# Kernel optimization log

Hardware: AMD Instinct MI355X
Metric: run time of the kernel (lower is better)

## Reference

```python
import jax, jax.numpy as jnp
import numpy as np

B, S, DIN, DOUT = 4, 2048, 4096, 4096

def setup_inputs() -> dict:
    key = jax.random.key(0)
    k1, k2, k3, k4 = jax.random.split(key, 4)
    x = jax.random.normal(k1, (B, S, DIN), dtype=jnp.float32)
    # symmetric int8 weight values in [-127, 127]
    quantized_weight = jax.random.randint(k2, (DOUT, DIN), -127, 128, dtype=jnp.int32).astype(jnp.int8)
    weight_scale = jax.random.uniform(k3, (), dtype=jnp.float32) * 0.01 + 1e-4
    bias = jax.random.normal(k4, (DOUT,), dtype=jnp.float32)
    return {"x": x, "quantized_weight": quantized_weight, "weight_scale": weight_scale, "bias": bias}

def reference(x, quantized_weight, weight_scale, bias) -> jnp.ndarray:
    # dequantize_tensor: (q.float() - 0) * scale
    weight_fp32 = quantized_weight.astype(jnp.float32) * weight_scale  # [DOUT, DIN]
    # nn.functional.linear: x @ W^T + b
    return jnp.einsum('bsi,oi->bso', x, weight_fp32) + bias
```

## Files before the change

kernel.cpp:

```cpp
#include <hip/hip_runtime.h>
#include <stdint.h>
#include <stddef.h>

constexpr int MDIM = 8192;
constexpr int NDIM = 4096;
constexpr int KDIM = 4096;

using f32x4 = __attribute__((ext_vector_type(4))) float;
using s16x4 = __attribute__((ext_vector_type(4))) short;
using s16x8 = __attribute__((ext_vector_type(8))) short;
using i32x4 = __attribute__((ext_vector_type(4))) int;

__device__ __forceinline__ short f32_to_bf16_rn(float f) {
  union { float f; uint32_t u; } v; v.f = f;
  uint32_t r = (v.u + 0x7FFFu + ((v.u >> 16) & 1u)) >> 16;
  return (short)(uint16_t)r;
}

__global__ void __launch_bounds__(256) quant_x_kernel(const float* __restrict__ in,
                                                      signed char* __restrict__ out,
                                                      float* __restrict__ sx) {
  const int row = blockIdx.x;
  const int t   = threadIdx.x;
  const float* rp = in + (size_t)row * KDIM;
  f32x4 v[4];
  float m = 0.0f;
#pragma unroll
  for (int j = 0; j < 4; ++j) {
    v[j] = *(const f32x4*)(rp + t * 16 + j * 4);
#pragma unroll
    for (int e = 0; e < 4; ++e) m = fmaxf(m, __builtin_fabsf(v[j][e]));
  }
#pragma unroll
  for (int off = 32; off > 0; off >>= 1) m = fmaxf(m, __shfl_xor(m, off, 64));
  __shared__ float wmax[4];
  const int wv = t >> 6, ln = t & 63;
  if (ln == 0) wmax[wv] = m;
  __syncthreads();
  m = fmaxf(fmaxf(wmax[0], wmax[1]), fmaxf(wmax[2], wmax[3]));
  const float inv = (m > 0.0f) ? (127.0f / m) : 0.0f;
  if (t == 0) sx[row] = m * (1.0f / 127.0f);
  i32x4 o;
#pragma unroll
  for (int j = 0; j < 4; ++j) {
    int b[4];
#pragma unroll
    for (int e = 0; e < 4; ++e) {
      int q = (int)rintf(v[j][e] * inv);
      q = q < -127 ? -127 : (q > 127 ? 127 : q);
      b[e] = q & 255;
    }
    o[j] = b[0] | (b[1] << 8) | (b[2] << 16) | (b[3] << 24);
  }
  *(i32x4*)(out + (size_t)row * KDIM + t * 16) = o;
}

__global__ void __launch_bounds__(256) quant_w_kernel(const int* __restrict__ in,
                                                      signed char* __restrict__ out, int n16) {
  int i = blockIdx.x * 256 + threadIdx.x;
  const int stride = gridDim.x * 256;
  for (; i < n16; i += stride) {
    const i32x4* p = (const i32x4*)(in + (size_t)i * 16);
    i32x4 o;
#pragma unroll
    for (int j = 0; j < 4; ++j) {
      i32x4 a = p[j];
      o[j] = (a[0] & 255) | ((a[1] & 255) << 8) | ((a[2] & 255) << 16) | ((a[3] & 255) << 24);
    }
    *(i32x4*)(out + (size_t)i * 16) = o;
  }
}


#define BAR asm volatile("s_barrier" ::: "memory")
#define WAITVM(n) asm volatile("s_waitcnt vmcnt(" #n ")" ::: "memory")

#define GLL(src, dst) __builtin_amdgcn_global_load_lds(                     \
    (const __attribute__((address_space(1))) void*)(src),                   \
    (__attribute__((address_space(3))) void*)(dst), 16, 0, 0)

#define STGP(tau) do {                                                      \
  GLL(Arow + (size_t)r0 * 4096 + (tau) * 64 + cb,                           \
      lds + (tau) * 32768 + t * 16);                                        \
  GLL(Arow + (size_t)(128 + r0) * 4096 + (tau) * 64 + cb,                   \
      lds + (tau) * 32768 + 8192 + t * 16);                                 \
  GLL(Brow + (size_t)r0 * 4096 + (tau) * 64 + cb,                           \
      lds + (tau) * 32768 + 16384 + t * 16);                                \
  GLL(Brow + (size_t)(128 + r0) * 4096 + (tau) * 64 + cb,                   \
      lds + (tau) * 32768 + 16384 + 8192 + t * 16);                         \
} while (0)

#define STGL(u3) do {                                                       \
  GLL(aSrc0, lds + (u3) * 32768 + t * 16);                                  \
  GLL(aSrc1, lds + (u3) * 32768 + 8192 + t * 16);                           \
  GLL(bSrc0, lds + (u3) * 32768 + 16384 + t * 16);                          \
  GLL(bSrc1, lds + (u3) * 32768 + 16384 + 8192 + t * 16);                   \
  aSrc0 += 64; aSrc1 += 64; bSrc0 += 64; bSrc1 += 64;                       \
} while (0)

#define LDA8(u, fi) (*(const i32x4*)(lds + (u) * 32768                      \
    + (wm * 8 + (fi)) * 1024 + laneoff))
#define LDB8(u, j)  (*(const i32x4*)(lds + (u) * 32768 + 16384              \
    + (wn * 4 + (j)) * 1024 + laneoff))

#define WIN(u, AFC, BFC, AFN, BFN, dord, dostg, vmarg) do {                 \
  if (dord) {                                                               \
    _Pragma("unroll") for (int i_ = 0; i_ < 8; ++i_)                        \
      AFN[i_] = LDA8(((u) + 1) & 3, i_);                                    \
    _Pragma("unroll") for (int j_ = 0; j_ < 4; ++j_)                        \
      BFN[j_] = LDB8(((u) + 1) & 3, j_);                                    \
  }                                                                         \
  if (dostg) STGL(((u) + 3) & 3);                                           \
  __builtin_amdgcn_s_setprio(1);                                            \
  _Pragma("unroll") for (int i_ = 0; i_ < 8; ++i_)                          \
  _Pragma("unroll") for (int j_ = 0; j_ < 4; ++j_)                          \
    acc[i_][j_] = __builtin_amdgcn_mfma_i32_16x16x64_i8(                    \
        AFC[i_], BFC[j_], acc[i_][j_], 0, 0, 0);                            \
  __builtin_amdgcn_s_setprio(0);                                            \
  if ((vmarg) == 4) { WAITVM(4); } else if ((vmarg) == 0) { WAITVM(0); }    \
  BAR;                                                                      \
} while (0)

__global__ void __launch_bounds__(512, 1) gemm_i8_ring(
    const signed char* __restrict__ A, const signed char* __restrict__ Bw,
    const float* __restrict__ sx, const float* __restrict__ scale_p,
    const float* __restrict__ bias, float* __restrict__ out) {
  __shared__ __align__(16) char lds[131072];

  const int t      = threadIdx.x;
  const int lane   = t & 63;
  const int wave   = t >> 6;
  const int wm     = wave >> 2;
  const int wn     = wave & 3;
  const int lane15 = lane & 15;
  const int lh     = lane >> 4;

  const int laneoff = (lane15 * 64 + lh * 16) ^ ((lane15 & 8) << 2);

  const int ax = ((t >> 5) & 1) << 5;
  const int a0 = (t * 16) ^ ax;
  const int r0 = a0 >> 6;
  const int cb = a0 & 63;

  const int bid   = blockIdx.x;
  const int wg    = (bid & 7) * 64 + (bid >> 3);
  const int ntile = wg & 15;
  const int mtile = wg >> 4;
  const int m0 = mtile * 256;
  const int n0 = ntile * 256;

  const char* Arow = (const char*)(A + (size_t)m0 * KDIM);
  const char* Brow = (const char*)(Bw + (size_t)n0 * KDIM);

  const char* aSrc0 = Arow + (size_t)r0 * 4096 + 192 + cb;
  const char* aSrc1 = Arow + (size_t)(128 + r0) * 4096 + 192 + cb;
  const char* bSrc0 = Brow + (size_t)r0 * 4096 + 192 + cb;
  const char* bSrc1 = Brow + (size_t)(128 + r0) * 4096 + 192 + cb;

  i32x4 acc[8][4] = {};
  i32x4 afE[8], afO[8], bfE[4], bfO[4];

  STGP(0);
  STGP(1);
  STGP(2);
  WAITVM(8);
  BAR;
#pragma unroll
  for (int i_ = 0; i_ < 8; ++i_) afE[i_] = LDA8(0, i_);
#pragma unroll
  for (int j_ = 0; j_ < 4; ++j_) bfE[j_] = LDB8(0, j_);
  WAITVM(4);
  BAR;

#pragma unroll 1
  for (int tp = 0; tp < 15; ++tp) {
    WIN(0, afE, bfE, afO, bfO, 1, 1, 4);
    WIN(1, afO, bfO, afE, bfE, 1, 1, 4);
    WIN(2, afE, bfE, afO, bfO, 1, 1, 4);
    WIN(3, afO, bfO, afE, bfE, 1, 1, 4);
  }
  WIN(0, afE, bfE, afO, bfO, 1, 1, 4);
  WIN(1, afO, bfO, afE, bfE, 1, 0, 0);
  WIN(2, afE, bfE, afO, bfO, 1, 0, -1);
  WIN(3, afO, bfO, afE, bfE, 0, 0, -1);

  const float sw = scale_p[0];
  float bv[4];
#pragma unroll
  for (int j = 0; j < 4; ++j) bv[j] = bias[n0 + wn * 64 + j * 16 + lane15];
#pragma unroll
  for (int i = 0; i < 8; ++i) {
    const int rowb = m0 + wm * 128 + i * 16 + lh * 4;
    float sxq[4];
#pragma unroll
    for (int q = 0; q < 4; ++q) sxq[q] = sx[rowb + q] * sw;
#pragma unroll
    for (int j = 0; j < 4; ++j) {
      const int col = n0 + wn * 64 + j * 16 + lane15;
#pragma unroll
      for (int q = 0; q < 4; ++q)
        out[(size_t)(rowb + q) * NDIM + col] = (float)acc[i][j][q] * sxq[q] + bv[j];
    }
  }
}

constexpr int FTILE = 128;
constexpr int FBK   = 64;

__global__ void __launch_bounds__(256) gemm_raw(
    const float* __restrict__ X, const int* __restrict__ W,
    const float* __restrict__ scale_p, const float* __restrict__ bias,
    float* __restrict__ out) {
  __shared__ short As[FTILE * FBK];
  __shared__ short Bs[FTILE * FBK];

  const int t      = threadIdx.x;
  const int lane   = t & 63;
  const int wave   = t >> 6;
  const int wm     = wave >> 1;
  const int wn     = wave & 1;
  const int lane15   = lane & 15;
  const int laneHalf = lane >> 4;

  const int bid   = blockIdx.x;
  const int wg    = (bid & 7) * 256 + (bid >> 3);
  const int ntile = wg & 31;
  const int mtile = wg >> 5;
  const int m0 = mtile * FTILE;
  const int n0 = ntile * FTILE;

  f32x4 acc[4][4] = {};

  for (int k0 = 0; k0 < KDIM; k0 += FBK) {
    __syncthreads();
#pragma unroll
    for (int r = 0; r < 8; ++r) {
      const int f   = r * 256 + t;
      const int row = f >> 4;
      const int c4  = (f & 15) * 4;
      f32x4 v = *(const f32x4*)(X + (size_t)(m0 + row) * KDIM + (k0 + c4));
      s16x4 h;
#pragma unroll
      for (int j = 0; j < 4; ++j) h[j] = f32_to_bf16_rn(v[j]);
      *(s16x4*)&As[row * FBK + c4] = h;

      i32x4 wv = *(const i32x4*)(W + (size_t)(n0 + row) * KDIM + (k0 + c4));
      s16x4 hw;
#pragma unroll
      for (int j = 0; j < 4; ++j) hw[j] = f32_to_bf16_rn((float)wv[j]);
      *(s16x4*)&Bs[row * FBK + c4] = hw;
    }
    __syncthreads();

#pragma unroll
    for (int kk = 0; kk < FBK; kk += 32) {
      const int kb = kk + laneHalf * 8;
      s16x8 af[4], bf[4];
#pragma unroll
      for (int i = 0; i < 4; ++i) {
        af[i] = *(const s16x8*)&As[(wm * 64 + i * 16 + lane15) * FBK + kb];
        bf[i] = *(const s16x8*)&Bs[(wn * 64 + i * 16 + lane15) * FBK + kb];
      }
#pragma unroll
      for (int i = 0; i < 4; ++i)
#pragma unroll
        for (int j = 0; j < 4; ++j)
          acc[i][j] = __builtin_amdgcn_mfma_f32_16x16x32_bf16(af[i], bf[j], acc[i][j], 0, 0, 0);
    }
  }

  const float s = scale_p[0];
#pragma unroll
  for (int j = 0; j < 4; ++j) {
    const int col = n0 + wn * 64 + j * 16 + lane15;
    const float bv = bias[col];
#pragma unroll
    for (int i = 0; i < 4; ++i) {
      const int row = m0 + wm * 64 + i * 16 + laneHalf * 4;
#pragma unroll
      for (int q = 0; q < 4; ++q)
        out[(size_t)(row + q) * NDIM + col] = acc[i][j][q] * s + bv;
    }
  }
}

extern "C" void kernel_launch(void* const* d_in, const int* in_sizes, int n_in,
                              void* d_out, int out_size, void* d_ws, size_t ws_size,
                              hipStream_t stream) {
  const float* x     = (const float*)d_in[0];
  const int*   w     = (const int*)d_in[1];
  const float* scale = (const float*)d_in[2];
  const float* bias  = (const float*)d_in[3];
  float* out = (float*)d_out;

  const size_t a_bytes = (size_t)MDIM * KDIM;
  const size_t b_bytes = (size_t)NDIM * KDIM;
  const size_t need    = a_bytes + b_bytes + MDIM * 4;

  if (ws_size >= need) {
    signed char* Ai8 = (signed char*)d_ws;
    signed char* Bi8 = Ai8 + a_bytes;
    float*       sxp = (float*)(Bi8 + b_bytes);
    quant_x_kernel<<<MDIM, 256, 0, stream>>>(x, Ai8, sxp);
    quant_w_kernel<<<4096, 256, 0, stream>>>(w, Bi8, (int)(b_bytes / 16));
    const int nwg = (MDIM / 256) * (NDIM / 256);
    gemm_i8_ring<<<nwg, 512, 0, stream>>>(Ai8, Bi8, sxp, scale, bias, out);
  } else {
    const int nwg = (MDIM / FTILE) * (NDIM / FTILE);
    gemm_raw<<<nwg, 256, 0, stream>>>(x, w, scale, bias, out);
  }
}
```

Before: 186.8 us.

## Switch int8 GEMM to 32x32x32 MFMA with new LDS swizzle layout

Replaces the 16x16x64 int8 MFMA tiling with 32x32x32 int8 MFMA, so each wave computes a 4x2 grid of 32x32 fragments with i32x16 accumulators split over two K sub-steps. The LDS staging addresses and XOR swizzle are redone for 32-row fragments, and the epilogue is rewritten for the 32x32 output register layout. The intent is fewer MFMA issues and fewer LDS fragment reads per unit of work, at the cost of a different bank-conflict pattern and a scattered epilogue store order.

```diff
diff --git a/kernel.cpp b/kernel.cpp
--- a/kernel.cpp
+++ b/kernel.cpp
@@ -6,10 +6,11 @@
 constexpr int NDIM = 4096;
 constexpr int KDIM = 4096;
 
-using f32x4 = __attribute__((ext_vector_type(4))) float;
-using s16x4 = __attribute__((ext_vector_type(4))) short;
-using s16x8 = __attribute__((ext_vector_type(8))) short;
-using i32x4 = __attribute__((ext_vector_type(4))) int;
+using f32x4  = __attribute__((ext_vector_type(4)))  float;
+using s16x4  = __attribute__((ext_vector_type(4)))  short;
+using s16x8  = __attribute__((ext_vector_type(8)))  short;
+using i32x4  = __attribute__((ext_vector_type(4)))  int;
+using i32x16 = __attribute__((ext_vector_type(16))) int;
 
 __device__ __forceinline__ short f32_to_bf16_rn(float f) {
   union { float f; uint32_t u; } v; v.f = f;
@@ -98,30 +99,35 @@
   aSrc0 += 64; aSrc1 += 64; bSrc0 += 64; bSrc1 += 64;                       \
 } while (0)
 
-#define LDA8(u, fi) (*(const i32x4*)(lds + (u) * 32768                      \
-    + (wm * 8 + (fi)) * 1024 + laneoff))
-#define LDB8(u, j)  (*(const i32x4*)(lds + (u) * 32768 + 16384              \
-    + (wn * 4 + (j)) * 1024 + laneoff))
+#define LDA32(u, fi, ks) (*(const i32x4*)(lds + (u) * 32768                 \
+    + wm * 8192 + (fi) * 2048 + ((ks) ? loffK1 : loffK0)))
+#define LDB32(u, fj, ks) (*(const i32x4*)(lds + (u) * 32768 + 16384         \
+    + wn * 4096 + (fj) * 2048 + ((ks) ? loffK1 : loffK0)))
 
 #define WIN(u, AFC, BFC, AFN, BFN, dord, dostg, vmarg) do {                 \
   if (dord) {                                                               \
-    _Pragma("unroll") for (int i_ = 0; i_ < 8; ++i_)                        \
-      AFN[i_] = LDA8(((u) + 1) & 3, i_);                                    \
-    _Pragma("unroll") for (int j_ = 0; j_ < 4; ++j_)                        \
-      BFN[j_] = LDB8(((u) + 1) & 3, j_);                                    \
+    _Pragma("unroll") for (int i_ = 0; i_ < 4; ++i_) {                      \
+      AFN[i_ * 2]     = LDA32(((u) + 1) & 3, i_, 0);                        \
+      AFN[i_ * 2 + 1] = LDA32(((u) + 1) & 3, i_, 1);                        \
+    }                                                                       \
+    _Pragma("unroll") for (int j_ = 0; j_ < 2; ++j_) {                      \
+      BFN[j_ * 2]     = LDB32(((u) + 1) & 3, j_, 0);                        \
+      BFN[j_ * 2 + 1] = LDB32(((u) + 1) & 3, j_, 1);                        \
+    }                                                                       \
   }                                                                         \
   if (dostg) STGL(((u) + 3) & 3);                                           \
   __builtin_amdgcn_s_setprio(1);                                            \
-  _Pragma("unroll") for (int i_ = 0; i_ < 8; ++i_)                          \
-  _Pragma("unroll") for (int j_ = 0; j_ < 4; ++j_)                          \
-    acc[i_][j_] = __builtin_amdgcn_mfma_i32_16x16x64_i8(                    \
-        AFC[i_], BFC[j_], acc[i_][j_], 0, 0, 0);                            \
+  _Pragma("unroll") for (int ks_ = 0; ks_ < 2; ++ks_)                       \
+  _Pragma("unroll") for (int i_ = 0; i_ < 4; ++i_)                          \
+  _Pragma("unroll") for (int j_ = 0; j_ < 2; ++j_)                          \
+    acc[i_][j_] = __builtin_amdgcn_mfma_i32_32x32x32_i8(                    \
+        AFC[i_ * 2 + ks_], BFC[j_ * 2 + ks_], acc[i_][j_], 0, 0, 0);        \
   __builtin_amdgcn_s_setprio(0);                                            \
   if ((vmarg) == 4) { WAITVM(4); } else if ((vmarg) == 0) { WAITVM(0); }    \
   BAR;                                                                      \
 } while (0)
 
-__global__ void __launch_bounds__(512, 1) gemm_i8_ring(
+__global__ void __launch_bounds__(512, 1) gemm_i8_ring32(
     const signed char* __restrict__ A, const signed char* __restrict__ Bw,
     const float* __restrict__ sx, const float* __restrict__ scale_p,
     const float* __restrict__ bias, float* __restrict__ out) {
@@ -132,15 +138,14 @@
   const int wave   = t >> 6;
   const int wm     = wave >> 2;
   const int wn     = wave & 3;
-  const int lane15 = lane & 15;
-  const int lh     = lane >> 4;
-
-  const int laneoff = (lane15 * 64 + lh * 16) ^ ((lane15 & 8) << 2);
-
-  const int ax = ((t >> 5) & 1) << 5;
-  const int a0 = (t * 16) ^ ax;
-  const int r0 = a0 >> 6;
-  const int cb = a0 & 63;
+  const int l31    = lane & 31;
+  const int lh     = lane >> 5;
+
+  const int loffK0 = l31 * 64 + ((lh)     ^ (l31 & 3)) * 16;
+  const int loffK1 = l31 * 64 + ((2 + lh) ^ (l31 & 3)) * 16;
+
+  const int r0 = t >> 2;
+  const int cb = (((t & 3) ^ ((t >> 2) & 3)) << 4);
 
   const int bid   = blockIdx.x;
   const int wg    = (bid & 7) * 64 + (bid >> 3);
@@ -157,7 +162,7 @@
   const char* bSrc0 = Brow + (size_t)r0 * 4096 + 192 + cb;
   const char* bSrc1 = Brow + (size_t)(128 + r0) * 4096 + 192 + cb;
 
-  i32x4 acc[8][4] = {};
+  i32x16 acc[4][2] = {};
   i32x4 afE[8], afO[8], bfE[4], bfO[4];
 
   STGP(0);
@@ -166,9 +171,15 @@
   WAITVM(8);
   BAR;
 #pragma unroll
-  for (int i_ = 0; i_ < 8; ++i_) afE[i_] = LDA8(0, i_);
-#pragma unroll
-  for (int j_ = 0; j_ < 4; ++j_) bfE[j_] = LDB8(0, j_);
+  for (int i_ = 0; i_ < 4; ++i_) {
+    afE[i_ * 2]     = LDA32(0, i_, 0);
+    afE[i_ * 2 + 1] = LDA32(0, i_, 1);
+  }
+#pragma unroll
+  for (int j_ = 0; j_ < 2; ++j_) {
+    bfE[j_ * 2]     = LDB32(0, j_, 0);
+    bfE[j_ * 2 + 1] = LDB32(0, j_, 1);
+  }
   WAITVM(4);
   BAR;
 
@@ -185,21 +196,21 @@
   WIN(3, afO, bfO, afE, bfE, 0, 0, -1);
 
   const float sw = scale_p[0];
-  float bv[4];
-#pragma unroll
-  for (int j = 0; j < 4; ++j) bv[j] = bias[n0 + wn * 64 + j * 16 + lane15];
-#pragma unroll
-  for (int i = 0; i < 8; ++i) {
-    const int rowb = m0 + wm * 128 + i * 16 + lh * 4;
-    float sxq[4];
-#pragma unroll
-    for (int q = 0; q < 4; ++q) sxq[q] = sx[rowb + q] * sw;
-#pragma unroll
-    for (int j = 0; j < 4; ++j) {
-      const int col = n0 + wn * 64 + j * 16 + lane15;
-#pragma unroll
-      for (int q = 0; q < 4; ++q)
-        out[(size_t)(rowb + q) * NDIM + col] = (float)acc[i][j][q] * sxq[q] + bv[j];
+  float bv[2];
+#pragma unroll
+  for (int j = 0; j < 2; ++j) bv[j] = bias[n0 + wn * 64 + j * 32 + l31];
+#pragma unroll
+  for (int fi = 0; fi < 4; ++fi) {
+    const int rowbase = m0 + wm * 128 + fi * 32 + lh * 4;
+#pragma unroll
+    for (int reg = 0; reg < 16; ++reg) {
+      const int row = rowbase + (reg & 3) + ((reg >> 2) << 3);
+      const float sxr = sx[row] * sw;
+#pragma unroll
+      for (int j = 0; j < 2; ++j) {
+        const int col = n0 + wn * 64 + j * 32 + l31;
+        out[(size_t)row * NDIM + col] = (float)acc[fi][j][reg] * sxr + bv[j];
+      }
     }
   }
 }
@@ -304,7 +315,7 @@
     quant_x_kernel<<<MDIM, 256, 0, stream>>>(x, Ai8, sxp);
     quant_w_kernel<<<4096, 256, 0, stream>>>(w, Bi8, (int)(b_bytes / 16));
     const int nwg = (MDIM / 256) * (NDIM / 256);
-    gemm_i8_ring<<<nwg, 512, 0, stream>>>(Ai8, Bi8, sxp, scale, bias, out);
+    gemm_i8_ring32<<<nwg, 512, 0, stream>>>(Ai8, Bi8, sxp, scale, bias, out);
   } else {
     const int nwg = (MDIM / FTILE) * (NDIM / FTILE);
     gemm_raw<<<nwg, 256, 0, stream>>>(x, w, scale, bias, out);
```

After: 213.5 us. 1.14x slower.
